# Optimization experiments

Hardware: AMD Instinct MI355X
Metric: run time of the kernel (lower is better)

## Reference

```python
import jax, jax.numpy as jnp
import numpy as np

N_EMB = 512
EMB_DIM = 64
COMMITMENT_COST = 0.25


def setup_inputs() -> dict:
    key = jax.random.key(0)
    k1, k2 = jax.random.split(key)
    x = jax.random.normal(k1, (32, 64, 64, EMB_DIM), dtype=jnp.float32)
    init_bound = 1.0 / N_EMB
    embedding = jax.random.uniform(k2, (N_EMB, EMB_DIM), dtype=jnp.float32,
                                   minval=-init_bound, maxval=init_bound)
    return {"x": x, "embedding": embedding}


def reference(x, embedding):
    M, D = embedding.shape
    x_flat = jax.lax.stop_gradient(x).reshape(-1, D)  # [N, D]
    # distances = (-cdist(x, E))**2 == squared euclidean distance; argmin identical
    # to argmin over cdist, computed without forming sqrt:
    d2 = (jnp.sum(x_flat * x_flat, axis=-1, keepdims=True)
          - 2.0 * (x_flat @ embedding.T)
          + jnp.sum(embedding * embedding, axis=-1))  # [N, M]
    indices = jnp.argmin(d2, axis=-1)  # [N]
    quantized = embedding[indices].reshape(x.shape)  # gather, view_as(x)

    # eval-mode (not training): commitment loss + straight-through estimator
    e_latent_loss = jnp.mean((x - jax.lax.stop_gradient(quantized)) ** 2)
    loss = COMMITMENT_COST * e_latent_loss
    quantized_st = x + jax.lax.stop_gradient(quantized - x)

    # perplexity from codebook usage (avg one-hot probabilities)
    counts = jnp.zeros((M,), dtype=jnp.float32).at[indices].add(1.0)
    avg_probs = counts / x_flat.shape[0]
    perplexity = jnp.exp(-jnp.sum(avg_probs * jnp.log(avg_probs + 1e-10)))
    return quantized_st, loss, perplexity
```

## Files before the change

### kernel.cpp

```cpp
#include <hip/hip_runtime.h>


#define D      64
#define M      512
#define N_VEC  131072
#define N_ELEM 8388608

typedef __attribute__((ext_vector_type(8))) short short8;
typedef __attribute__((ext_vector_type(4))) float f32x4;


static __device__ __forceinline__ unsigned short f2bf(float f) {
    unsigned u = __float_as_uint(f);
    return (unsigned short)((u + 0x7FFFu + ((u >> 16) & 1u)) >> 16);
}

__global__ __launch_bounds__(256)
void vq_prep(const float* __restrict__ emb, float* __restrict__ bnorm,
             unsigned short* __restrict__ planes, float* __restrict__ loss_sum,
             unsigned* __restrict__ ticket, unsigned* __restrict__ ghist) {
    const int g = blockIdx.x * 256 + threadIdx.x;
    if (g == 0) { *loss_sum = 0.f; *ticket = 0u; }
    if (g < M) ghist[g] = 0u;

    const int c = g >> 3, s = (g >> 2) & 1, q = g & 3;
    const float* e = emb + c * D + s * 32 + q * 8;
    short8 h;
#pragma unroll
    for (int j = 0; j < 8; ++j) h[j] = (short)f2bf(e[j]);
    const int ct = c >> 4, col = c & 15;
    *(short8*)(planes + ((ct * 2 + s) * 64 + q * 16 + col) * 8) = h;

    if ((g & 7) == 0) {
        const float* ec = emb + c * D;
        float s0 = 0.f, s1 = 0.f, s2 = 0.f, s3 = 0.f;
        for (int k = 0; k < D; k += 4) {
            float e0 = ec[k], e1 = ec[k + 1], e2 = ec[k + 2], e3 = ec[k + 3];
            s0 = fmaf(e0, e0, s0); s1 = fmaf(e1, e1, s1);
            s2 = fmaf(e2, e2, s2); s3 = fmaf(e3, e3, s3);
        }
        bnorm[c] = 1.0f + ((s0 + s1) + (s2 + s3));
    }
}

__global__ __launch_bounds__(512, 4)
void vq_main(const float* __restrict__ x, const float* __restrict__ emb,
             const float* __restrict__ bnorm, const unsigned short* __restrict__ planes,
             float* __restrict__ out, float* __restrict__ loss_sum,
             unsigned* __restrict__ ticket, unsigned* __restrict__ ghist) {
    __shared__ __align__(16) short sE[32768];
    __shared__ float sBn[M];
    __shared__ unsigned sCode[256];
    __shared__ unsigned sHist[M];
    __shared__ float sRed[8];
    __shared__ unsigned sLast;

    const int tid = threadIdx.x;
    const int w = tid >> 6, lane = tid & 63;
    const int q = lane >> 4, col = lane & 15;
    const int rowBase = blockIdx.x * 256 + w * 32;

    {
        const short8* src = (const short8*)planes;
        short8* dst = (short8*)sE;
#pragma unroll
        for (int k = 0; k < 8; ++k) dst[tid + k * 512] = src[tid + k * 512];
        sBn[tid] = bnorm[tid];
        sHist[tid] = 0u;
    }

    float4 xc[8];
    {
        const float* p0 = x + (size_t)(rowBase + col) * D + q * 8;
        const float* p1 = x + (size_t)(rowBase + 16 + col) * D + q * 8;
        xc[0] = *(const float4*)(p0);      xc[1] = *(const float4*)(p0 + 4);
        xc[2] = *(const float4*)(p0 + 32); xc[3] = *(const float4*)(p0 + 36);
        xc[4] = *(const float4*)(p1);      xc[5] = *(const float4*)(p1 + 4);
        xc[6] = *(const float4*)(p1 + 32); xc[7] = *(const float4*)(p1 + 36);
    }

    short8 XH[2][2];
#pragma unroll
    for (int p = 0; p < 2; ++p) {
        float f[16] = {xc[p*4+0].x, xc[p*4+0].y, xc[p*4+0].z, xc[p*4+0].w,
                       xc[p*4+1].x, xc[p*4+1].y, xc[p*4+1].z, xc[p*4+1].w,
                       xc[p*4+2].x, xc[p*4+2].y, xc[p*4+2].z, xc[p*4+2].w,
                       xc[p*4+3].x, xc[p*4+3].y, xc[p*4+3].z, xc[p*4+3].w};
#pragma unroll
        for (int j = 0; j < 8; ++j) {
            XH[p][0][j] = (short)f2bf(f[j]);
            XH[p][1][j] = (short)f2bf(f[8 + j]);
        }
    }

    __syncthreads();

    unsigned best0 = 0xFFFFFFFFu, best1 = 0xFFFFFFFFu;
#pragma unroll 4
    for (int t = 0; t < 32; ++t) {
        const int fb = t * 1024 + lane * 8;
        short8 Eh0 = *(const short8*)&sE[fb];
        short8 Eh1 = *(const short8*)&sE[fb + 512];
        f32x4 Bn4 = *(const f32x4*)&sBn[t * 16 + q * 4];

        f32x4 a1 = {0.f, 0.f, 0.f, 0.f};
        a1 = __builtin_amdgcn_mfma_f32_16x16x32_bf16(Eh0, XH[0][0], a1, 0, 0, 0);
        a1 = __builtin_amdgcn_mfma_f32_16x16x32_bf16(Eh1, XH[0][1], a1, 0, 0, 0);
        f32x4 b1 = {0.f, 0.f, 0.f, 0.f};
        b1 = __builtin_amdgcn_mfma_f32_16x16x32_bf16(Eh0, XH[1][0], b1, 0, 0, 0);
        b1 = __builtin_amdgcn_mfma_f32_16x16x32_bf16(Eh1, XH[1][1], b1, 0, 0, 0);

        const int cb = t * 16 + q * 4;
#pragma unroll
        for (int r = 0; r < 4; ++r) {
            float sc0 = fmaf(-2.0f, a1[r], Bn4[r]);
            float sc1 = fmaf(-2.0f, b1[r], Bn4[r]);
            unsigned p0 = (__float_as_uint(sc0) & 0xFFFFFE00u) | (unsigned)(cb + r);
            unsigned p1 = (__float_as_uint(sc1) & 0xFFFFFE00u) | (unsigned)(cb + r);
            best0 = p0 < best0 ? p0 : best0;
            best1 = p1 < best1 ? p1 : best1;
        }
    }

    {
        unsigned o;
        o = __shfl_xor(best0, 16, 64); best0 = o < best0 ? o : best0;
        o = __shfl_xor(best0, 32, 64); best0 = o < best0 ? o : best0;
        o = __shfl_xor(best1, 16, 64); best1 = o < best1 ? o : best1;
        o = __shfl_xor(best1, 32, 64); best1 = o < best1 ? o : best1;
    }
    if (q == 0) {
        const unsigned c0 = best0 & 511u, c1 = best1 & 511u;
        sCode[w * 32 + col] = c0;
        sCode[w * 32 + 16 + col] = c1;
        atomicAdd(&sHist[c0], 1u);
        atomicAdd(&sHist[c1], 1u);
    }

    float lacc = 0.f;
#pragma unroll 2
    for (int i = 0; i < 8; ++i) {
        const int rr = i * 4 + q;
        const unsigned code = sCode[w * 32 + rr];
        const size_t a = (size_t)(rowBase + rr) * D + col * 4;
        const float4 xv = *(const float4*)(x + a);
        const float4 qv = *(const float4*)(emb + (size_t)code * D + col * 4);
        const float e0 = xv.x - qv.x, e1 = xv.y - qv.y, e2 = xv.z - qv.z, e3 = xv.w - qv.w;
        lacc = fmaf(e0, e0, lacc); lacc = fmaf(e1, e1, lacc);
        lacc = fmaf(e2, e2, lacc); lacc = fmaf(e3, e3, lacc);
        float4 o;
        o.x = xv.x - e0; o.y = xv.y - e1; o.z = xv.z - e2; o.w = xv.w - e3;
        *(float4*)(out + a) = o;
    }
#pragma unroll
    for (int off = 32; off > 0; off >>= 1) lacc += __shfl_down(lacc, off, 64);
    if (lane == 0) sRed[w] = lacc;
    __syncthreads();

    {
        const unsigned h = sHist[tid];
        if (h) atomicAdd(&ghist[tid], h);
    }
    if (tid == 0) {
        float s = ((sRed[0] + sRed[1]) + (sRed[2] + sRed[3]))
                + ((sRed[4] + sRed[5]) + (sRed[6] + sRed[7]));
        atomicAdd(loss_sum, s);
    }
    __syncthreads();

    if (tid == 0) {
        __threadfence();
        sLast = (atomicAdd(ticket, 1u) == 511u) ? 1u : 0u;
    }
    __syncthreads();

    if (sLast) {
        const unsigned cnt = atomicAdd(&ghist[tid], 0u);
        const float p = (float)cnt * (1.0f / 131072.0f);
        float term = p * logf(p + 1e-10f);
#pragma unroll
        for (int off = 32; off > 0; off >>= 1) term += __shfl_down(term, off, 64);
        if (lane == 0) sRed[w] = term;
        __syncthreads();
        if (tid == 0) {
            float s = 0.f;
#pragma unroll
            for (int ww = 0; ww < 8; ++ww) s += sRed[ww];
            const float L = atomicAdd(loss_sum, 0.0f);
            out[N_ELEM]     = 0.25f * (L * (1.0f / 8388608.0f));
            out[N_ELEM + 1] = expf(-s);
        }
    }
}

extern "C" void kernel_launch(void* const* d_in, const int* in_sizes, int n_in,
                              void* d_out, int out_size, void* d_ws, size_t ws_size,
                              hipStream_t stream) {
    (void)in_sizes; (void)n_in; (void)out_size; (void)ws_size;
    const float* x   = (const float*)d_in[0];
    const float* emb = (const float*)d_in[1];
    float* out = (float*)d_out;

    float*          loss   = (float*)d_ws;
    unsigned*       ticket = (unsigned*)((char*)d_ws + 32);
    float*          bnorm  = (float*)((char*)d_ws + 64);
    unsigned short* plns   = (unsigned short*)((char*)d_ws + 4096);
    unsigned*       ghist  = (unsigned*)((char*)d_ws + 131072);

    vq_prep<<<dim3(16), dim3(256), 0, stream>>>(emb, bnorm, plns, loss, ticket, ghist);
    vq_main<<<dim3(512), dim3(512), 0, stream>>>(x, emb, bnorm, plns, out, loss,
                                                 ticket, ghist);
}
```

Before: 113.4 us.

## Fuse codebook prep into main kernel and shard global histogram atomics

Drops the separate prep kernel. Each block now converts the fp32 codebook to bf16 MFMA planes and computes codebook norms directly into shared memory, and a hipMemsetAsync zeroes the workspace. The global histogram is split into 8 copies indexed by block to reduce atomic contention, and the last block sums the copies. This removes one kernel launch and its dependency, but every block now repeats the conversion work and a memset node is added.

```diff
diff --git a/kernel.cpp b/kernel.cpp
--- a/kernel.cpp
+++ b/kernel.cpp
@@ -15,37 +15,8 @@
     return (unsigned short)((u + 0x7FFFu + ((u >> 16) & 1u)) >> 16);
 }
 
-__global__ __launch_bounds__(256)
-void vq_prep(const float* __restrict__ emb, float* __restrict__ bnorm,
-             unsigned short* __restrict__ planes, float* __restrict__ loss_sum,
-             unsigned* __restrict__ ticket, unsigned* __restrict__ ghist) {
-    const int g = blockIdx.x * 256 + threadIdx.x;
-    if (g == 0) { *loss_sum = 0.f; *ticket = 0u; }
-    if (g < M) ghist[g] = 0u;
-
-    const int c = g >> 3, s = (g >> 2) & 1, q = g & 3;
-    const float* e = emb + c * D + s * 32 + q * 8;
-    short8 h;
-#pragma unroll
-    for (int j = 0; j < 8; ++j) h[j] = (short)f2bf(e[j]);
-    const int ct = c >> 4, col = c & 15;
-    *(short8*)(planes + ((ct * 2 + s) * 64 + q * 16 + col) * 8) = h;
-
-    if ((g & 7) == 0) {
-        const float* ec = emb + c * D;
-        float s0 = 0.f, s1 = 0.f, s2 = 0.f, s3 = 0.f;
-        for (int k = 0; k < D; k += 4) {
-            float e0 = ec[k], e1 = ec[k + 1], e2 = ec[k + 2], e3 = ec[k + 3];
-            s0 = fmaf(e0, e0, s0); s1 = fmaf(e1, e1, s1);
-            s2 = fmaf(e2, e2, s2); s3 = fmaf(e3, e3, s3);
-        }
-        bnorm[c] = 1.0f + ((s0 + s1) + (s2 + s3));
-    }
-}
-
 __global__ __launch_bounds__(512, 4)
 void vq_main(const float* __restrict__ x, const float* __restrict__ emb,
-             const float* __restrict__ bnorm, const unsigned short* __restrict__ planes,
              float* __restrict__ out, float* __restrict__ loss_sum,
              unsigned* __restrict__ ticket, unsigned* __restrict__ ghist) {
     __shared__ __align__(16) short sE[32768];
@@ -61,12 +32,31 @@
     const int rowBase = blockIdx.x * 256 + w * 32;
 
     {
-        const short8* src = (const short8*)planes;
-        short8* dst = (short8*)sE;
-#pragma unroll
-        for (int k = 0; k < 8; ++k) dst[tid + k * 512] = src[tid + k * 512];
-        sBn[tid] = bnorm[tid];
-        sHist[tid] = 0u;
+        const int c = tid, ct = c >> 4, ccol = c & 15;
+        float s0 = 0.f, s1 = 0.f, s2 = 0.f, s3 = 0.f;
+#pragma unroll
+        for (int s = 0; s < 2; ++s) {
+            float4 v[8];
+#pragma unroll
+            for (int m = 0; m < 8; ++m)
+                v[m] = *(const float4*)(emb + c * D + s * 32 + m * 4);
+#pragma unroll
+            for (int m = 0; m < 8; ++m) {
+                s0 = fmaf(v[m].x, v[m].x, s0); s1 = fmaf(v[m].y, v[m].y, s1);
+                s2 = fmaf(v[m].z, v[m].z, s2); s3 = fmaf(v[m].w, v[m].w, s3);
+            }
+#pragma unroll
+            for (int qq = 0; qq < 4; ++qq) {
+                const float ff[8] = {v[qq*2].x, v[qq*2].y, v[qq*2].z, v[qq*2].w,
+                                     v[qq*2+1].x, v[qq*2+1].y, v[qq*2+1].z, v[qq*2+1].w};
+                short8 h;
+#pragma unroll
+                for (int j = 0; j < 8; ++j) h[j] = (short)f2bf(ff[j]);
+                *(short8*)&sE[(((ct * 2 + s) * 64) + qq * 16 + ccol) * 8] = h;
+            }
+        }
+        sBn[c] = 1.0f + ((s0 + s1) + (s2 + s3));
+        sHist[c] = 0u;
     }
 
     float4 xc[8];
@@ -159,7 +149,7 @@
 
     {
         const unsigned h = sHist[tid];
-        if (h) atomicAdd(&ghist[tid], h);
+        if (h) atomicAdd(&ghist[((unsigned)blockIdx.x & 7u) * 512u + tid], h);
     }
     if (tid == 0) {
         float s = ((sRed[0] + sRed[1]) + (sRed[2] + sRed[3]))
@@ -175,7 +165,9 @@
     __syncthreads();
 
     if (sLast) {
-        const unsigned cnt = atomicAdd(&ghist[tid], 0u);
+        unsigned cnt = 0;
+#pragma unroll
+        for (int k = 0; k < 8; ++k) cnt += atomicAdd(&ghist[k * 512 + tid], 0u);
         const float p = (float)cnt * (1.0f / 131072.0f);
         float term = p * logf(p + 1e-10f);
 #pragma unroll
@@ -201,13 +193,11 @@
     const float* emb = (const float*)d_in[1];
     float* out = (float*)d_out;
 
-    float*          loss   = (float*)d_ws;
-    unsigned*       ticket = (unsigned*)((char*)d_ws + 32);
-    float*          bnorm  = (float*)((char*)d_ws + 64);
-    unsigned short* plns   = (unsigned short*)((char*)d_ws + 4096);
-    unsigned*       ghist  = (unsigned*)((char*)d_ws + 131072);
-
-    vq_prep<<<dim3(16), dim3(256), 0, stream>>>(emb, bnorm, plns, loss, ticket, ghist);
-    vq_main<<<dim3(512), dim3(512), 0, stream>>>(x, emb, bnorm, plns, out, loss,
-                                                 ticket, ghist);
+    float*    loss   = (float*)d_ws;
+    unsigned* ticket = (unsigned*)((char*)d_ws + 32);
+    unsigned* ghist  = (unsigned*)((char*)d_ws + 64);
+
+    hipMemsetAsync(d_ws, 0, 64 + 8 * 512 * sizeof(unsigned), stream);
+
+    vq_main<<<dim3(512), dim3(512), 0, stream>>>(x, emb, out, loss, ticket, ghist);
 }
```

Result: slower. 117.1 us (+3.2%).
